# Optimization experiments

Measured on AMD Instinct MI355X. Metric: run time of the kernel, lower is better.

Reference implementation:

```python
import jax, jax.numpy as jnp
import numpy as np

B, T, D, H = 4096, 512, 25, 25
NUM_LAYERS = 3


def setup_inputs() -> dict:
    key = jax.random.key(0)
    ks = jax.random.split(key, 9)
    s = 1.0 / np.sqrt(H)  # torch LSTM/Linear default init scale
    return {
        "x": jax.random.normal(ks[0], (B, T, D), dtype=jnp.float32),
        "Wih": jax.random.uniform(ks[1], (NUM_LAYERS, 4 * H, D), minval=-s, maxval=s),
        "Whh": jax.random.uniform(ks[2], (NUM_LAYERS, 4 * H, H), minval=-s, maxval=s),
        "bih": jax.random.uniform(ks[3], (NUM_LAYERS, 4 * H), minval=-s, maxval=s),
        "bhh": jax.random.uniform(ks[4], (NUM_LAYERS, 4 * H), minval=-s, maxval=s),
        "W1": jax.random.uniform(ks[5], (16, H), minval=-s, maxval=s),
        "b1": jax.random.uniform(ks[6], (16,), minval=-s, maxval=s),
        "W2": jax.random.uniform(ks[7], (14, 16), minval=-0.25, maxval=0.25),
        "b2": jax.random.uniform(ks[8], (14,), minval=-0.25, maxval=0.25),
    }


def _lstm_layer(x, Wih, Whh, b):
    """Single LSTM layer, batch_first. x: [B,T,Din] -> hs: [B,T,H].
    Torch gate order: i, f, g, o."""
    # Precompute input contribution for all timesteps at once: [B,T,4H]
    xg = jnp.einsum('btd,gd->btg', x, Wih) + b

    def step(carry, xg_t):
        h, c = carry
        g = xg_t + h @ Whh.T  # [B,4H]
        i, f, gg, o = jnp.split(g, 4, axis=-1)
        c = jax.nn.sigmoid(f) * c + jax.nn.sigmoid(i) * jnp.tanh(gg)
        h = jax.nn.sigmoid(o) * jnp.tanh(c)
        return (h, c), h

    h0 = jnp.zeros((x.shape[0], H), x.dtype)
    (_, _), hs = jax.lax.scan(step, (h0, h0), jnp.swapaxes(xg, 0, 1))  # [T,B,H]
    return jnp.swapaxes(hs, 0, 1)


def reference(x, Wih, Whh, bih, bhh, W1, b1, W2, b2):
    h = x
    for l in range(NUM_LAYERS):  # eval mode: inter-layer dropout disabled
        h = _lstm_layer(h, Wih[l], Whh[l], bih[l] + bhh[l])
    last = h[:, -1, :]                       # [B,H]
    out = jax.nn.relu(last @ W1.T + b1)      # [B,16]
    return jax.nn.softmax(out @ W2.T + b2, axis=1)  # [B,14]
```

## Files before the change

kernel.cpp:

```cpp
#include <hip/hip_runtime.h>


#define NBATCH 4096
#define NT     512
#define ND     25
#define NG     100
#define NL     3

__device__ __forceinline__ float sigf(float x) {
    return __builtin_amdgcn_rcpf(1.0f + __expf(-x));
}
__device__ __forceinline__ float tanhfast(float x) {
    float s = sigf(x + x);
    return s + s - 1.0f;
}

__global__ __launch_bounds__(256, 4)
void lstm2(const float* __restrict__ xin,
           const float* __restrict__ Wih,
           const float* __restrict__ Whh,
           const float* __restrict__ bih,
           const float* __restrict__ bhh,
           const float* __restrict__ W1,
           const float* __restrict__ b1,
           const float* __restrict__ W2,
           const float* __restrict__ b2,
           float* __restrict__ out,
           float* __restrict__ ws)
{
    __shared__ __align__(16) float xh[2][56];
    __shared__ float act[2][112];

    const int wid  = threadIdx.x >> 6;
    const int lane = threadIdx.x & 63;
    const int wb   = wid >> 1;
    const int role = wid & 1;
    const int b    = (blockIdx.x << 1) + wb;

    const int  lrow    = (lane < 50) ? lane : 49;
    const bool updater = (role == 0) && (lane < 25);

    float w[52];
    w[50] = 0.f; w[51] = 0.f;

    for (int l = 0; l < NL; ++l) {
        const int row = l * NG + role * 50 + lrow;
        const float* wihp = Wih + row * ND;
        const float* whhp = Whh + row * ND;
#pragma unroll
        for (int d = 0; d < 25; ++d) { w[d] = wihp[d]; w[25 + d] = whhp[d]; }
        const float bias = bih[row] + bhh[row];

        const float* src = (l == 0) ? (xin + (size_t)b * NT * ND)
                                    : (ws  + (size_t)b * NT * ND);
        float* wsrow = ws + (size_t)b * NT * ND;

        float c = 0.f;
        float xv_next = 0.f;
        if (updater) {
            xh[wb][lane] = src[lane];
            xv_next = src[ND + lane];
        }
        if (role == 0 && lane < 31) xh[wb][25 + lane] = 0.f;
        __syncthreads();

        for (int t = 0; t < NT; ++t) {
            float acc = bias;
#pragma unroll
            for (int c4 = 0; c4 < 13; ++c4) {
                const float4 v = *(const float4*)&xh[wb][c4 * 4];
                acc = fmaf(w[c4 * 4 + 0], v.x, acc);
                acc = fmaf(w[c4 * 4 + 1], v.y, acc);
                acc = fmaf(w[c4 * 4 + 2], v.z, acc);
                acc = fmaf(w[c4 * 4 + 3], v.w, acc);
            }
            float a;
            if (role == 0) a = sigf(acc);
            else           a = (lane < 25) ? tanhfast(acc)
                                           : sigf(acc);
            if (lane < 50) act[wb][role * 56 + lane] = a;
            __syncthreads();

            if (updater) {
                const float ig = act[wb][lane];
                const float fg = act[wb][25 + lane];
                const float gg = act[wb][56 + lane];
                const float og = act[wb][81 + lane];
                c = fmaf(fg, c, ig * gg);
                const float h = og * tanhfast(c);
                xh[wb][25 + lane] = h;
                xh[wb][lane]      = xv_next;
                if (l < 2) wsrow[t * ND + lane] = h;
                if (t + 2 < NT) xv_next = src[(t + 2) * ND + lane];
            }
            __syncthreads();
        }
    }

    if (role == 0 && lane < 16) {
        float u = b1[lane];
#pragma unroll
        for (int d = 0; d < 25; ++d) u = fmaf(W1[lane * 25 + d], xh[wb][25 + d], u);
        act[wb][lane] = fmaxf(u, 0.f);
    }
    if (role == 0 && lane < 14) {
        float lg = b2[lane];
#pragma unroll
        for (int r = 0; r < 16; ++r) lg = fmaf(W2[lane * 16 + r], act[wb][r], lg);
        act[wb][32 + lane] = lg;
    }
    if (role == 0 && lane < 14) {
        float m = -1e30f;
#pragma unroll
        for (int j = 0; j < 14; ++j) m = fmaxf(m, act[wb][32 + j]);
        float sum = 0.f;
#pragma unroll
        for (int j = 0; j < 14; ++j) sum += __expf(act[wb][32 + j] - m);
        out[b * 14 + lane] = __expf(act[wb][32 + lane] - m) / sum;
    }
}

extern "C" void kernel_launch(void* const* d_in, const int* in_sizes, int n_in,
                              void* d_out, int out_size, void* d_ws, size_t ws_size,
                              hipStream_t stream)
{
    const float* x   = (const float*)d_in[0];
    const float* Wih = (const float*)d_in[1];
    const float* Whh = (const float*)d_in[2];
    const float* bih = (const float*)d_in[3];
    const float* bhh = (const float*)d_in[4];
    const float* W1  = (const float*)d_in[5];
    const float* b1  = (const float*)d_in[6];
    const float* W2  = (const float*)d_in[7];
    const float* b2  = (const float*)d_in[8];
    float* outp = (float*)d_out;
    float* ws   = (float*)d_ws;

    dim3 grid(NBATCH / 2), block(256);
    hipLaunchKernelGGL(lstm2, grid, block, 0, stream,
                       x, Wih, Whh, bih, bhh, W1, b1, W2, b2, outp, ws);
}
```

Before: 1.884 ms.

## Replicate LSTM state update per wave and drop second barrier per step

```diff
diff --git a/kernel.cpp b/kernel.cpp
--- a/kernel.cpp
+++ b/kernel.cpp
@@ -15,8 +15,8 @@
     return s + s - 1.0f;
 }
 
-__global__ __launch_bounds__(256, 4)
-void lstm2(const float* __restrict__ xin,
+__global__ __launch_bounds__(256, 3)
+void lstm3(const float* __restrict__ xin,
            const float* __restrict__ Wih,
            const float* __restrict__ Whh,
            const float* __restrict__ bih,
@@ -28,8 +28,8 @@
            float* __restrict__ out,
            float* __restrict__ ws)
 {
-    __shared__ __align__(16) float xh[2][56];
-    __shared__ float act[2][112];
+    __shared__ __align__(16) float xh[2][2][56];
+    __shared__ float act[2][2][112];
 
     const int wid  = threadIdx.x >> 6;
     const int lane = threadIdx.x & 63;
@@ -37,8 +37,8 @@
     const int role = wid & 1;
     const int b    = (blockIdx.x << 1) + wb;
 
-    const int  lrow    = (lane < 50) ? lane : 49;
-    const bool updater = (role == 0) && (lane < 25);
+    const int lrow = (lane < 50) ? lane : 49;
+    float* const myxh = xh[wb][role];
 
     float w[52];
     w[50] = 0.f; w[51] = 0.f;
@@ -56,67 +56,69 @@
         float* wsrow = ws + (size_t)b * NT * ND;
 
         float c = 0.f;
-        float xv_next = 0.f;
-        if (updater) {
-            xh[wb][lane] = src[lane];
-            xv_next = src[ND + lane];
-        }
-        if (role == 0 && lane < 31) xh[wb][25 + lane] = 0.f;
+        if (lane < 25)                    myxh[lane] = src[lane];
+        else if (lane < 56)               myxh[lane] = 0.f;
+        float xv_next = (lane < 25) ? src[ND + lane] : 0.f;
         __syncthreads();
 
         for (int t = 0; t < NT; ++t) {
-            float acc = bias;
+            const int p = t & 1;
+            float a0 = bias, a1 = 0.f, a2 = 0.f, a3 = 0.f;
 #pragma unroll
             for (int c4 = 0; c4 < 13; ++c4) {
-                const float4 v = *(const float4*)&xh[wb][c4 * 4];
-                acc = fmaf(w[c4 * 4 + 0], v.x, acc);
-                acc = fmaf(w[c4 * 4 + 1], v.y, acc);
-                acc = fmaf(w[c4 * 4 + 2], v.z, acc);
-                acc = fmaf(w[c4 * 4 + 3], v.w, acc);
+                const float4 v = *(const float4*)&myxh[c4 * 4];
+                a0 = fmaf(w[c4 * 4 + 0], v.x, a0);
+                a1 = fmaf(w[c4 * 4 + 1], v.y, a1);
+                a2 = fmaf(w[c4 * 4 + 2], v.z, a2);
+                a3 = fmaf(w[c4 * 4 + 3], v.w, a3);
             }
+            const float acc = (a0 + a1) + (a2 + a3);
+
             float a;
             if (role == 0) a = sigf(acc);
             else           a = (lane < 25) ? tanhfast(acc)
                                            : sigf(acc);
-            if (lane < 50) act[wb][role * 56 + lane] = a;
+            if (lane < 50) act[wb][p][role * 56 + lane] = a;
             __syncthreads();
 
-            if (updater) {
-                const float ig = act[wb][lane];
-                const float fg = act[wb][25 + lane];
-                const float gg = act[wb][56 + lane];
-                const float og = act[wb][81 + lane];
+            if (lane < 25) {
+                const float ig = act[wb][p][lane];
+                const float fg = act[wb][p][25 + lane];
+                const float gg = act[wb][p][56 + lane];
+                const float og = act[wb][p][81 + lane];
                 c = fmaf(fg, c, ig * gg);
                 const float h = og * tanhfast(c);
-                xh[wb][25 + lane] = h;
-                xh[wb][lane]      = xv_next;
-                if (l < 2) wsrow[t * ND + lane] = h;
+                myxh[25 + lane] = h;
+                myxh[lane]      = xv_next;
+                if (role == 0 && l < 2) wsrow[t * ND + lane] = h;
                 if (t + 2 < NT) xv_next = src[(t + 2) * ND + lane];
             }
-            __syncthreads();
         }
     }
 
-    if (role == 0 && lane < 16) {
-        float u = b1[lane];
+    if (role == 0) {
+        float* sc = act[wb][0];
+        if (lane < 16) {
+            float u = b1[lane];
 #pragma unroll
-        for (int d = 0; d < 25; ++d) u = fmaf(W1[lane * 25 + d], xh[wb][25 + d], u);
-        act[wb][lane] = fmaxf(u, 0.f);
-    }
-    if (role == 0 && lane < 14) {
-        float lg = b2[lane];
+            for (int d = 0; d < 25; ++d) u = fmaf(W1[lane * 25 + d], myxh[25 + d], u);
+            sc[lane] = fmaxf(u, 0.f);
+        }
+        if (lane < 14) {
+            float lg = b2[lane];
 #pragma unroll
-        for (int r = 0; r < 16; ++r) lg = fmaf(W2[lane * 16 + r], act[wb][r], lg);
-        act[wb][32 + lane] = lg;
-    }
-    if (role == 0 && lane < 14) {
-        float m = -1e30f;
+            for (int r = 0; r < 16; ++r) lg = fmaf(W2[lane * 16 + r], sc[r], lg);
+            sc[32 + lane] = lg;
+        }
+        if (lane < 14) {
+            float m = -1e30f;
 #pragma unroll
-        for (int j = 0; j < 14; ++j) m = fmaxf(m, act[wb][32 + j]);
-        float sum = 0.f;
+            for (int j = 0; j < 14; ++j) m = fmaxf(m, sc[32 + j]);
+            float sum = 0.f;
 #pragma unroll
-        for (int j = 0; j < 14; ++j) sum += __expf(act[wb][32 + j] - m);
-        out[b * 14 + lane] = __expf(act[wb][32 + lane] - m) / sum;
+            for (int j = 0; j < 14; ++j) sum += __expf(sc[32 + j] - m);
+            out[b * 14 + lane] = __expf(sc[32 + lane] - m) / sum;
+        }
     }
 }
 
@@ -137,6 +139,6 @@
     float* ws   = (float*)d_ws;
 
     dim3 grid(NBATCH / 2), block(256);
-    hipLaunchKernelGGL(lstm2, grid, block, 0, stream,
+    hipLaunchKernelGGL(lstm3, grid, block, 0, stream,
                        x, Wih, Whh, bih, bhh, W1, b1, W2, b2, outp, ws);
 }
```

Result: no change. 1.907 ms (+1.2%).

## Map one batch element per half-wavefront with all four gates per lane

Applied to the files above, without the earlier changes.

```diff
diff --git a/kernel.cpp b/kernel.cpp
--- a/kernel.cpp
+++ b/kernel.cpp
@@ -1,122 +1,153 @@
 #include <hip/hip_runtime.h>
 
 
-#define NBATCH 4096
-#define NT     512
-#define ND     25
-#define NG     100
-#define NL     3
+typedef float f32x2 __attribute__((ext_vector_type(2)));
+typedef float f32x4 __attribute__((ext_vector_type(4)));
 
-__device__ __forceinline__ float sigf(float x) {
-    return __builtin_amdgcn_rcpf(1.0f + __expf(-x));
-}
-__device__ __forceinline__ float tanhfast(float x) {
-    float s = sigf(x + x);
-    return s + s - 1.0f;
+#define NT 512
+#define ND 25
+
+__device__ __forceinline__ float exp2f_(float x){ return __builtin_amdgcn_exp2f(x); }
+__device__ __forceinline__ float rcpf_(float x){ return __builtin_amdgcn_rcpf(x); }
+__device__ __forceinline__ float sigf(float x){ return rcpf_(1.f + exp2f_(-1.442695041f*x)); }
+__device__ __forceinline__ float tanhf_(float x){ return fmaf(2.f, rcpf_(1.f + exp2f_(-2.885390082f*x)), -1.f); }
+
+__device__ __forceinline__ f32x2 mkw(const float* wi, const float* wh, int m){
+    const int j0 = 2*m, j1 = 2*m + 1;
+    const float e0 = (j0 < ND) ? wi[j0] : wh[j0 - ND];
+    const float e1 = (j1 < ND) ? wi[j1] : wh[j1 - ND];
+    return (f32x2){e0, e1};
 }
 
-__global__ __launch_bounds__(256, 4)
-void lstm2(const float* __restrict__ xin,
+#define LO2(v) __builtin_shufflevector(v, v, 0, 1)
+#define HI2(v) __builtin_shufflevector(v, v, 2, 3)
+
+#define M25(F) F(0) F(1) F(2) F(3) F(4) F(5) F(6) F(7) F(8) F(9) F(10) F(11) F(12) \
+               F(13) F(14) F(15) F(16) F(17) F(18) F(19) F(20) F(21) F(22) F(23) F(24)
+
+#define WDEF(m) f32x2 wI##m = mkw(wiI, whI, m), wF##m = mkw(wiF, whF, m), \
+                      wG##m = mkw(wiG, whG, m), wO##m = mkw(wiO, whO, m);
+
+#define PK4(m, V) \
+    aI = __builtin_elementwise_fma(wI##m, V, aI); \
+    aF = __builtin_elementwise_fma(wF##m, V, aF); \
+    aG = __builtin_elementwise_fma(wG##m, V, aG); \
+    aO = __builtin_elementwise_fma(wO##m, V, aO);
+
+__global__ __launch_bounds__(256, 2)
+void lstm8(const float* __restrict__ xin,
            const float* __restrict__ Wih,
            const float* __restrict__ Whh,
            const float* __restrict__ bih,
            const float* __restrict__ bhh,
-           const float* __restrict__ W1,
-           const float* __restrict__ b1,
-           const float* __restrict__ W2,
-           const float* __restrict__ b2,
+           const float* __restrict__ W1p,
+           const float* __restrict__ b1p,
+           const float* __restrict__ W2p,
+           const float* __restrict__ b2p,
            float* __restrict__ out,
            float* __restrict__ ws)
 {
-    __shared__ __align__(16) float xh[2][56];
-    __shared__ float act[2][112];
+    __shared__ __align__(16) float vec[4][2][56];
 
     const int wid  = threadIdx.x >> 6;
     const int lane = threadIdx.x & 63;
-    const int wb   = wid >> 1;
-    const int role = wid & 1;
-    const int b    = (blockIdx.x << 1) + wb;
+    const int half = lane >> 5;
+    const int u    = lane & 31;
+    const int uc   = (u < ND) ? u : ND - 1;
+    const bool act_ = (u < ND);
+    const int b    = (blockIdx.x * 4 + wid) * 2 + half;
 
-    const int  lrow    = (lane < 50) ? lane : 49;
-    const bool updater = (role == 0) && (lane < 25);
+    float* const myvec = &vec[wid][half][0];
+    const f32x4* const vv = (const f32x4*)myvec;
 
-    float w[52];
-    w[50] = 0.f; w[51] = 0.f;
+    float hlast = 0.f;
 
-    for (int l = 0; l < NL; ++l) {
-        const int row = l * NG + role * 50 + lrow;
-        const float* wihp = Wih + row * ND;
-        const float* whhp = Whh + row * ND;
-#pragma unroll
-        for (int d = 0; d < 25; ++d) { w[d] = wihp[d]; w[25 + d] = whhp[d]; }
-        const float bias = bih[row] + bhh[row];
+    for (int l = 0; l < 3; ++l) {
+        const int rI = l * 100 + uc;
+        const float* wiI = Wih + (size_t)rI * ND;        const float* whI = Whh + (size_t)rI * ND;
+        const float* wiF = Wih + (size_t)(rI + 25) * ND; const float* whF = Whh + (size_t)(rI + 25) * ND;
+        const float* wiG = Wih + (size_t)(rI + 50) * ND; const float* whG = Whh + (size_t)(rI + 50) * ND;
+        const float* wiO = Wih + (size_t)(rI + 75) * ND; const float* whO = Whh + (size_t)(rI + 75) * ND;
+        M25(WDEF)
+        const float bI = bih[rI]      + bhh[rI];
+        const float bF = bih[rI + 25] + bhh[rI + 25];
+        const float bG = bih[rI + 50] + bhh[rI + 50];
+        const float bO = bih[rI + 75] + bhh[rI + 75];
 
         const float* src = (l == 0) ? (xin + (size_t)b * NT * ND)
                                     : (ws  + (size_t)b * NT * ND);
-        float* wsrow = ws + (size_t)b * NT * ND;
+        const float* srcu = src + uc;
+        float* const wsb = ws + (size_t)b * NT * ND + uc;
 
-        float c = 0.f;
-        float xv_next = 0.f;
-        if (updater) {
-            xh[wb][lane] = src[lane];
-            xv_next = src[ND + lane];
-        }
-        if (role == 0 && lane < 31) xh[wb][25 + lane] = 0.f;
-        __syncthreads();
+        const float x0v = srcu[0];
+        if (act_) { myvec[u] = x0v; myvec[ND + u] = 0.f; }
+        float xn1 = srcu[ND];
+        float xn2 = srcu[2 * ND];
+        float c = 0.f, h = 0.f;
 
         for (int t = 0; t < NT; ++t) {
-            float acc = bias;
+            f32x2 aI = {bI, 0.f}, aF = {bF, 0.f}, aG = {bG, 0.f}, aO = {bO, 0.f};
+            f32x4 va = vv[0], vb = vv[1], vc2 = vv[2];
+            PK4(0,  LO2(va)) PK4(1,  HI2(va)) va  = vv[3];
+            PK4(2,  LO2(vb)) PK4(3,  HI2(vb)) vb  = vv[4];
+            PK4(4,  LO2(vc2)) PK4(5, HI2(vc2)) vc2 = vv[5];
+            PK4(6,  LO2(va)) PK4(7,  HI2(va)) va  = vv[6];
+            PK4(8,  LO2(vb)) PK4(9,  HI2(vb)) vb  = vv[7];
+            PK4(10, LO2(vc2)) PK4(11, HI2(vc2)) vc2 = vv[8];
+            PK4(12, LO2(va)) PK4(13, HI2(va)) va  = vv[9];
+            PK4(14, LO2(vb)) PK4(15, HI2(vb)) vb  = vv[10];
+            PK4(16, LO2(vc2)) PK4(17, HI2(vc2)) vc2 = vv[11];
+            PK4(18, LO2(va)) PK4(19, HI2(va)) va  = vv[12];
+            PK4(20, LO2(vb)) PK4(21, HI2(vb))
+            PK4(22, LO2(vc2)) PK4(23, HI2(vc2))
+            PK4(24, LO2(va))
+
+            const float si = sigf(aI.x + aI.y);
+            const float sf = sigf(aF.x + aF.y);
+            const float sg = tanhf_(aG.x + aG.y);
+            const float so = sigf(aO.x + aO.y);
+            c = fmaf(sf, c, si * sg);
+            h = so * tanhf_(c);
+
+            if (act_) {
+                myvec[ND + u] = h;
+                myvec[u]      = xn1;
+                if (l < 2) wsb[(size_t)t * ND] = h;
+            }
+            xn1 = xn2;
+            if (t + 3 < NT) xn2 = srcu[(size_t)(t + 3) * ND];
+        }
+
+        asm volatile("s_waitcnt vmcnt(0)" ::: "memory");
+        hlast = h;
+    }
+    (void)hlast;
+
+    {
+        const int r1 = (u < 16) ? u : 15;
+        float u1 = b1p[r1];
 #pragma unroll
-            for (int c4 = 0; c4 < 13; ++c4) {
-                const float4 v = *(const float4*)&xh[wb][c4 * 4];
-                acc = fmaf(w[c4 * 4 + 0], v.x, acc);
-                acc = fmaf(w[c4 * 4 + 1], v.y, acc);
-                acc = fmaf(w[c4 * 4 + 2], v.z, acc);
-                acc = fmaf(w[c4 * 4 + 3], v.w, acc);
-            }
-            float a;
-            if (role == 0) a = sigf(acc);
-            else           a = (lane < 25) ? tanhfast(acc)
-                                           : sigf(acc);
-            if (lane < 50) act[wb][role * 56 + lane] = a;
-            __syncthreads();
+        for (int d = 0; d < ND; ++d)
+            u1 = fmaf(W1p[r1 * ND + d], myvec[ND + d], u1);
+        u1 = fmaxf(u1, 0.f);
+        if (u < 16) myvec[u] = u1;
 
-            if (updater) {
-                const float ig = act[wb][lane];
-                const float fg = act[wb][25 + lane];
-                const float gg = act[wb][56 + lane];
-                const float og = act[wb][81 + lane];
-                c = fmaf(fg, c, ig * gg);
-                const float h = og * tanhfast(c);
-                xh[wb][25 + lane] = h;
-                xh[wb][lane]      = xv_next;
-                if (l < 2) wsrow[t * ND + lane] = h;
-                if (t + 2 < NT) xv_next = src[(t + 2) * ND + lane];
-            }
-            __syncthreads();
-        }
-    }
+        const int r2 = (u < 14) ? u : 13;
+        float lg = b2p[r2];
+#pragma unroll
+        for (int k = 0; k < 16; ++k)
+            lg = fmaf(W2p[r2 * 16 + k], myvec[k], lg);
+        if (u < 14) myvec[ND + u] = lg;
 
-    if (role == 0 && lane < 16) {
-        float u = b1[lane];
-#pragma unroll
-        for (int d = 0; d < 25; ++d) u = fmaf(W1[lane * 25 + d], xh[wb][25 + d], u);
-        act[wb][lane] = fmaxf(u, 0.f);
-    }
-    if (role == 0 && lane < 14) {
-        float lg = b2[lane];
-#pragma unroll
-        for (int r = 0; r < 16; ++r) lg = fmaf(W2[lane * 16 + r], act[wb][r], lg);
-        act[wb][32 + lane] = lg;
-    }
-    if (role == 0 && lane < 14) {
         float m = -1e30f;
 #pragma unroll
-        for (int j = 0; j < 14; ++j) m = fmaxf(m, act[wb][32 + j]);
-        float sum = 0.f;
+        for (int j = 0; j < 14; ++j) m = fmaxf(m, myvec[ND + j]);
+        float s = 0.f;
 #pragma unroll
-        for (int j = 0; j < 14; ++j) sum += __expf(act[wb][32 + j] - m);
-        out[b * 14 + lane] = __expf(act[wb][32 + lane] - m) / sum;
+        for (int j = 0; j < 14; ++j)
+            s += exp2f_(1.442695041f * (myvec[ND + j] - m));
+        const float pr = exp2f_(1.442695041f * (lg - m)) * rcpf_(s);
+        if (u < 14) out[b * 14 + u] = pr;
     }
 }
 
@@ -136,7 +167,7 @@
     float* outp = (float*)d_out;
     float* ws   = (float*)d_ws;
 
-    dim3 grid(NBATCH / 2), block(256);
-    hipLaunchKernelGGL(lstm2, grid, block, 0, stream,
+    dim3 grid(512), block(256);
+    hipLaunchKernelGGL(lstm8, grid, block, 0, stream,
                        x, Wih, Whh, bih, bhh, W1, b1, W2, b2, outp, ws);
 }
```

Result: slower. 3.109 ms (+65.0%).
